# Performance work log

Hardware: AMD Instinct MI355X
Metric: run time of the kernel (lower is better)

## Reference

```python
import jax, jax.numpy as jnp
import numpy as np

HIDDEN = 2048
NUM_HEADS = 16
KEY_DIM = 1024      # hidden * expand_k (0.5)
VALUE_DIM = 2048    # hidden * expand_v (1.0)
HEAD_K = KEY_DIM // NUM_HEADS   # 64
HEAD_V = VALUE_DIM // NUM_HEADS # 128
EPS = 1e-5
B, T = 8, 4096


def _rmsnorm(x, w, eps=EPS):
    var = jnp.mean(jnp.square(x), axis=-1, keepdims=True)
    return x * jax.lax.rsqrt(var + eps) * w


def setup_inputs() -> dict:
    key = jax.random.key(0)
    ks = jax.random.split(key, 7)
    s = 1.0 / np.sqrt(HIDDEN)
    return {
        "hidden_states": jax.random.normal(ks[0], (B, T, HIDDEN), dtype=jnp.float32),
        "recurrent_state": jax.random.normal(ks[1], (B, NUM_HEADS, HEAD_K, HEAD_V), dtype=jnp.float32),
        "norm_w": jnp.ones((HIDDEN,), dtype=jnp.float32),
        "q_w": jax.random.uniform(ks[2], (KEY_DIM, HIDDEN), jnp.float32, -s, s),
        "v_norm_w": jnp.ones((HEAD_V,), dtype=jnp.float32),
        "o_w": jax.random.uniform(ks[3], (HIDDEN, VALUE_DIM), jnp.float32, -s, s),
        "gate_w": jax.random.uniform(ks[4], (HIDDEN, HIDDEN), jnp.float32, -s, s),
    }


def reference(hidden_states, recurrent_state, norm_w, q_w, v_norm_w, o_w, gate_w):
    x = _rmsnorm(hidden_states, norm_w)                       # (B,T,D)
    q = x @ q_w.T                                             # (B,T,KEY_DIM)
    q = q.reshape(*q.shape[:2], NUM_HEADS, HEAD_K)            # (B,T,H,K)
    # L2 normalize along last dim (F.normalize default eps=1e-12 on the norm)
    norm = jnp.maximum(jnp.linalg.norm(q, axis=-1, keepdims=True), 1e-12)
    q = q / norm
    o = jnp.einsum('bthk,bhkv->bthv', q, recurrent_state)     # (B,T,H,V)
    o = _rmsnorm(o, v_norm_w)
    o = o.reshape(*o.shape[:2], VALUE_DIM)                    # (B,T,VALUE_DIM)
    o = o @ o_w.T                                             # (B,T,D)
    gate = jax.nn.sigmoid(x @ gate_w.T)                       # (B,T,D)
    return gate * o
```

## Files before the change

### kernel.cpp

```cpp
#include <hip/hip_runtime.h>

typedef unsigned short u16;
typedef unsigned int u32;
typedef __attribute__((ext_vector_type(4))) float f32x4;
typedef __attribute__((ext_vector_type(8))) short short8;
typedef __attribute__((ext_vector_type(4))) short short4v;

#define HIDDEN 2048
#define NHEADS 16
#define KEYDIM 1024
#define VALDIM 2048
#define HEADK 64
#define HEADV 128
#define NBATCH 8
#define SEQ 4096
#define NTOK (NBATCH * SEQ)

__device__ __forceinline__ u16 f2bf(float f) {
  union { float f; u32 u; } c; c.f = f;
  u32 r = c.u + 0x7FFFu + ((c.u >> 16) & 1u);
  return (u16)(r >> 16);
}
__device__ __forceinline__ float bf2f(u16 h) {
  union { u32 u; float f; } c; c.u = ((u32)h) << 16;
  return c.f;
}

__global__ __launch_bounds__(256) void cast_bf16_k(const float* __restrict__ in,
                                                   u16* __restrict__ out, int n4) {
  int i = blockIdx.x * blockDim.x + threadIdx.x;
  if (i >= n4) return;
  f32x4 v = *(const f32x4*)(in + (size_t)i * 4);
  short4v o;
  o[0] = (short)f2bf(v[0]); o[1] = (short)f2bf(v[1]);
  o[2] = (short)f2bf(v[2]); o[3] = (short)f2bf(v[3]);
  *(short4v*)(out + (size_t)i * 4) = o;
}

__global__ __launch_bounds__(256) void rmsnorm_cast_k(const float* __restrict__ x,
                                                      const float* __restrict__ w,
                                                      u16* __restrict__ xb) {
  int r = blockIdx.x;
  int tid = threadIdx.x;
  const float* xp = x + (size_t)r * HIDDEN + tid * 8;
  f32x4 v0 = *(const f32x4*)xp;
  f32x4 v1 = *(const f32x4*)(xp + 4);
  float ss = v0[0]*v0[0]+v0[1]*v0[1]+v0[2]*v0[2]+v0[3]*v0[3]
           + v1[0]*v1[0]+v1[1]*v1[1]+v1[2]*v1[2]+v1[3]*v1[3];
  #pragma unroll
  for (int m = 32; m >= 1; m >>= 1) ss += __shfl_xor(ss, m);
  __shared__ float red[4];
  if ((tid & 63) == 0) red[tid >> 6] = ss;
  __syncthreads();
  float tot = red[0] + red[1] + red[2] + red[3];
  float inv = rsqrtf(tot * (1.0f / HIDDEN) + 1e-5f);
  const float* wp = w + tid * 8;
  f32x4 w0 = *(const f32x4*)wp;
  f32x4 w1 = *(const f32x4*)(wp + 4);
  short8 o;
  o[0] = (short)f2bf(v0[0] * inv * w0[0]);
  o[1] = (short)f2bf(v0[1] * inv * w0[1]);
  o[2] = (short)f2bf(v0[2] * inv * w0[2]);
  o[3] = (short)f2bf(v0[3] * inv * w0[3]);
  o[4] = (short)f2bf(v1[0] * inv * w1[0]);
  o[5] = (short)f2bf(v1[1] * inv * w1[1]);
  o[6] = (short)f2bf(v1[2] * inv * w1[2]);
  o[7] = (short)f2bf(v1[3] * inv * w1[3]);
  *(short8*)(xb + (size_t)r * HIDDEN + tid * 8) = o;
}


__device__ __forceinline__ void gload16(const u16* g, u16* l) {
  __builtin_amdgcn_global_load_lds((const __attribute__((address_space(1))) void*)g,
                                   (__attribute__((address_space(3))) void*)l, 16, 0, 0);
}

#define BUF_U16 16384
#define NBUF 4

template <int MODE>
__global__ __launch_bounds__(512, 2) void gemm256_k(const u16* __restrict__ A,
                                                    const u16* __restrict__ Bw,
                                                    void* __restrict__ Cptr,
                                                    int M, int N, int K) {
  extern __shared__ u16 lds[];
  const int tid = threadIdx.x;
  const int wid = tid >> 6;
  const int wm = wid >> 2;
  const int wn = wid & 3;
  const int l = tid & 63;
  const int lr = l & 15;
  const int kq = l >> 4;

  const int ntn = N >> 8;
  const int per = gridDim.x >> 3;
  const int b = blockIdx.x;
  const int s = (b & 7) * per + (b >> 3);
  const int mt = s / ntn;
  const int nt = s - mt * ntn;

  const u16* Ag = A + (size_t)mt * 256 * K;
  const u16* Bg = Bw + (size_t)nt * 256 * K;

  const int srow = tid >> 2;
  const int kel = (((tid & 3) ^ ((tid >> 3) & 3)) << 3);
  u16* dA0 = lds + tid * 8;
  u16* dA1 = lds + (512 + tid) * 8;
  u16* dB0 = lds + 8192 + tid * 8;
  u16* dB1 = lds + 8192 + (512 + tid) * 8;

  const int NT = K >> 5;

#define STAGE(t)                                                        \
  do {                                                                  \
    int _off = (int)(((t) & 3) * BUF_U16);                              \
    int _k0 = (t) << 5;                                                 \
    const u16* _as = Ag + (size_t)srow * K + _k0 + kel;                 \
    gload16(_as, dA0 + _off);                                           \
    gload16(_as + (size_t)128 * K, dA1 + _off);                         \
    const u16* _bs = Bg + (size_t)srow * K + _k0 + kel;                 \
    gload16(_bs, dB0 + _off);                                           \
    gload16(_bs + (size_t)128 * K, dB1 + _off);                         \
  } while (0)

  STAGE(0);
  STAGE(1);
  STAGE(2);

  f32x4 acc[8][4] = {};

  for (int t = 0; t < NT; ++t) {
    if (t + 2 < NT)      asm volatile("s_waitcnt vmcnt(8)" ::: "memory");
    else if (t + 1 < NT) asm volatile("s_waitcnt vmcnt(4)" ::: "memory");
    else                 asm volatile("s_waitcnt vmcnt(0)" ::: "memory");
    __builtin_amdgcn_s_barrier();
    asm volatile("" ::: "memory");
    __builtin_amdgcn_sched_barrier(0);

    if (t + 3 < NT) STAGE(t + 3);

    const u16* bufA = lds + (size_t)(t & 3) * BUF_U16;
    const u16* bufB = bufA + 8192;

    short8 bfr[4], afr[8];
    #pragma unroll
    for (int n = 0; n < 4; ++n) {
      int R = wn * 64 + n * 16 + lr;
      bfr[n] = *(const short8*)(bufB + R * 32 + ((kq ^ ((R >> 1) & 3)) << 3));
    }
    #pragma unroll
    for (int m = 0; m < 8; ++m) {
      int R = wm * 128 + m * 16 + lr;
      afr[m] = *(const short8*)(bufA + R * 32 + ((kq ^ ((R >> 1) & 3)) << 3));
    }
    __builtin_amdgcn_s_setprio(1);
    #pragma unroll
    for (int m = 0; m < 8; ++m) {
      #pragma unroll
      for (int n = 0; n < 4; ++n)
        acc[m][n] = __builtin_amdgcn_mfma_f32_16x16x32_bf16(afr[m], bfr[n], acc[m][n], 0, 0, 0);
    }
    __builtin_amdgcn_s_setprio(0);
  }
#undef STAGE

  const int rowB = mt * 256 + wm * 128 + kq * 4;
  const int colB = nt * 256 + wn * 64 + lr;
  #pragma unroll
  for (int m = 0; m < 8; ++m) {
    #pragma unroll
    for (int n = 0; n < 4; ++n) {
      #pragma unroll
      for (int j = 0; j < 4; ++j) {
        int row = rowB + m * 16 + j;
        int col = colB + n * 16;
        size_t idx = (size_t)row * N + col;
        float v = acc[m][n][j];
        if constexpr (MODE == 0) {
          ((u16*)Cptr)[idx] = f2bf(v);
        } else if constexpr (MODE == 1) {
          ((float*)Cptr)[idx] = 1.0f / (1.0f + __expf(-v));
        } else {
          float* O = (float*)Cptr;
          O[idx] = O[idx] * v;
        }
      }
    }
  }
}

__global__ __launch_bounds__(256) void glaread_k(const u16* __restrict__ q,
                                                 const float* __restrict__ S,
                                                 const float* __restrict__ vw,
                                                 u16* __restrict__ omid) {
  int bh = blockIdx.x;
  int b = bh >> 4, h = bh & 15;
  int tid = threadIdx.x;
  int w = tid >> 6, l = tid & 63;
  int lr = l & 15, kq = l >> 4;

  const float* Sp = S + (size_t)bh * HEADK * HEADV;
  short8 bfrag[8][2];
  #pragma unroll
  for (int n = 0; n < 8; ++n) {
    #pragma unroll
    for (int s = 0; s < 2; ++s) {
      #pragma unroll
      for (int i = 0; i < 8; ++i)
        bfrag[n][s][i] =
            (short)f2bf(Sp[(size_t)(s * 32 + kq * 8 + i) * HEADV + n * 16 + lr]);
    }
  }
  float vwn[8];
  #pragma unroll
  for (int n = 0; n < 8; ++n) vwn[n] = vw[n * 16 + lr];

  #pragma unroll 1
  for (int it = 0; it < 8; ++it) {
    int t0 = blockIdx.y * 512 + it * 64 + w * 16;
    const u16* qp = q + (size_t)(b * SEQ + t0 + lr) * KEYDIM + h * HEADK;
    short8 a0 = *(const short8*)(qp + kq * 8);
    short8 a1 = *(const short8*)(qp + 32 + kq * 8);

    float ss = 0.f;
    #pragma unroll
    for (int i = 0; i < 8; ++i) {
      float x0 = bf2f((u16)a0[i]), x1 = bf2f((u16)a1[i]);
      ss += x0 * x0 + x1 * x1;
    }
    ss += __shfl_xor(ss, 16);
    ss += __shfl_xor(ss, 32);
    float sc = 1.0f / fmaxf(sqrtf(ss), 1e-12f);

    short8 an0, an1;
    #pragma unroll
    for (int i = 0; i < 8; ++i) {
      an0[i] = (short)f2bf(bf2f((u16)a0[i]) * sc);
      an1[i] = (short)f2bf(bf2f((u16)a1[i]) * sc);
    }

    f32x4 acc[8] = {};
    #pragma unroll
    for (int n = 0; n < 8; ++n) {
      acc[n] = __builtin_amdgcn_mfma_f32_16x16x32_bf16(an0, bfrag[n][0], acc[n], 0, 0, 0);
      acc[n] = __builtin_amdgcn_mfma_f32_16x16x32_bf16(an1, bfrag[n][1], acc[n], 0, 0, 0);
    }

    float part[4] = {0.f, 0.f, 0.f, 0.f};
    #pragma unroll
    for (int n = 0; n < 8; ++n) {
      #pragma unroll
      for (int j = 0; j < 4; ++j) part[j] += acc[n][j] * acc[n][j];
    }
    #pragma unroll
    for (int msk = 1; msk <= 8; msk <<= 1) {
      #pragma unroll
      for (int j = 0; j < 4; ++j) part[j] += __shfl_xor(part[j], msk);
    }
    #pragma unroll
    for (int j = 0; j < 4; ++j) {
      float inv = rsqrtf(part[j] * (1.0f / HEADV) + 1e-5f);
      int tok = t0 + kq * 4 + j;
      u16* op = omid + (size_t)(b * SEQ + tok) * VALDIM + h * HEADV;
      #pragma unroll
      for (int n = 0; n < 8; ++n)
        op[n * 16 + lr] = f2bf(acc[n][j] * inv * vwn[n]);
    }
  }
}

extern "C" void kernel_launch(void* const* d_in, const int* in_sizes, int n_in,
                              void* d_out, int out_size, void* d_ws, size_t ws_size,
                              hipStream_t stream) {
  const float* hs = (const float*)d_in[0];
  const float* S  = (const float*)d_in[1];
  const float* nw = (const float*)d_in[2];
  const float* qw = (const float*)d_in[3];
  const float* vw = (const float*)d_in[4];
  const float* ow = (const float*)d_in[5];
  const float* gw = (const float*)d_in[6];
  float* out = (float*)d_out;

  u16* xb   = (u16*)d_ws;
  u16* q    = xb + (size_t)NTOK * HIDDEN;
  u16* qwb  = q + (size_t)NTOK * KEYDIM;
  u16* owb  = qwb + (size_t)KEYDIM * HIDDEN;
  u16* gwb  = owb + (size_t)HIDDEN * VALDIM;
  u16* omid = xb;

  const size_t LDSB = (size_t)NBUF * BUF_U16 * sizeof(u16);

  cast_bf16_k<<<(KEYDIM * HIDDEN / 4 + 255) / 256, 256, 0, stream>>>(qw, qwb, KEYDIM * HIDDEN / 4);
  cast_bf16_k<<<(HIDDEN * VALDIM / 4 + 255) / 256, 256, 0, stream>>>(ow, owb, HIDDEN * VALDIM / 4);
  cast_bf16_k<<<(HIDDEN * HIDDEN / 4 + 255) / 256, 256, 0, stream>>>(gw, gwb, HIDDEN * HIDDEN / 4);

  rmsnorm_cast_k<<<NTOK, 256, 0, stream>>>(hs, nw, xb);

  gemm256_k<0><<<dim3((NTOK / 256) * (KEYDIM / 256)), 512, LDSB, stream>>>(xb, qwb, q, NTOK, KEYDIM, HIDDEN);

  gemm256_k<1><<<dim3((NTOK / 256) * (HIDDEN / 256)), 512, LDSB, stream>>>(xb, gwb, out, NTOK, HIDDEN, HIDDEN);

  glaread_k<<<dim3(NBATCH * NHEADS, SEQ / 512), 256, 0, stream>>>(q, S, vw, omid);

  gemm256_k<2><<<dim3((NTOK / 256) * (HIDDEN / 256)), 512, LDSB, stream>>>(omid, owb, out, NTOK, HIDDEN, VALDIM);
}
```

Baseline: 0.9999 ms.

## Restructure GEMM main loop into 8-phase ping-pong schedule with 64-wide K tiles

Replaces the 4-buffer, 32-wide-K GEMM pipeline with a two-buffer, 64-wide-K scheme. Each K=128 iteration is split into eight phases, each issuing one quarter of the LDS fragment loads and global-to-LDS prefetches and then a barrier-bracketed MFMA block. The goal is to interleave memory traffic with MFMA work in a fixed schedule, in the style of the HipKittens 8-wave pattern. LDS rises to 128KB per block, which likely limits occupancy to one block per CU despite launch_bounds(512,2), and the added barriers raise synchronisation overhead.

```diff
diff --git a/kernel.cpp b/kernel.cpp
--- a/kernel.cpp
+++ b/kernel.cpp
@@ -75,14 +75,17 @@
                                    (__attribute__((address_space(3))) void*)l, 16, 0, 0);
 }
 
-#define BUF_U16 16384
-#define NBUF 4
+#define BAR()                                  \
+  do {                                         \
+    __builtin_amdgcn_s_barrier();              \
+    __builtin_amdgcn_sched_barrier(0);         \
+  } while (0)
 
 template <int MODE>
-__global__ __launch_bounds__(512, 2) void gemm256_k(const u16* __restrict__ A,
-                                                    const u16* __restrict__ Bw,
-                                                    void* __restrict__ Cptr,
-                                                    int M, int N, int K) {
+__global__ __launch_bounds__(512, 2) void gemm8p_k(const u16* __restrict__ A,
+                                                   const u16* __restrict__ Bw,
+                                                   void* __restrict__ Cptr,
+                                                   int M, int N, int K) {
   extern __shared__ u16 lds[];
   const int tid = threadIdx.x;
   const int wid = tid >> 6;
@@ -95,74 +98,115 @@
   const int ntn = N >> 8;
   const int per = gridDim.x >> 3;
   const int b = blockIdx.x;
-  const int s = (b & 7) * per + (b >> 3);
-  const int mt = s / ntn;
-  const int nt = s - mt * ntn;
-
-  const u16* Ag = A + (size_t)mt * 256 * K;
-  const u16* Bg = Bw + (size_t)nt * 256 * K;
-
-  const int srow = tid >> 2;
-  const int kel = (((tid & 3) ^ ((tid >> 3) & 3)) << 3);
-  u16* dA0 = lds + tid * 8;
-  u16* dA1 = lds + (512 + tid) * 8;
-  u16* dB0 = lds + 8192 + tid * 8;
-  u16* dB1 = lds + 8192 + (512 + tid) * 8;
-
-  const int NT = K >> 5;
-
-#define STAGE(t)                                                        \
-  do {                                                                  \
-    int _off = (int)(((t) & 3) * BUF_U16);                              \
-    int _k0 = (t) << 5;                                                 \
-    const u16* _as = Ag + (size_t)srow * K + _k0 + kel;                 \
-    gload16(_as, dA0 + _off);                                           \
-    gload16(_as + (size_t)128 * K, dA1 + _off);                         \
-    const u16* _bs = Bg + (size_t)srow * K + _k0 + kel;                 \
-    gload16(_bs, dB0 + _off);                                           \
-    gload16(_bs + (size_t)128 * K, dB1 + _off);                         \
+  const int sidx = (b & 7) * per + (b >> 3);
+  const int mt = sidx / ntn;
+  const int nt = sidx - mt * ntn;
+
+  const u16* Ag = A + (size_t)(mt * 256) * K;
+  const u16* Bg = Bw + (size_t)(nt * 256) * K;
+
+  const int srow = tid >> 3;
+  const int schunk = (tid & 7) ^ (srow & 7);
+
+#define STAGE_A(c, h)                                                          \
+  do {                                                                         \
+    const u16* _s = Ag + (size_t)((h) * 128 + srow) * K + ((c) << 6) + schunk * 8; \
+    u16* _d = lds + (((c) & 1) << 15) + (h) * 8192 + tid * 8;                  \
+    gload16(_s, _d);                                                           \
+    gload16(_s + (size_t)64 * K, _d + 4096);                                   \
   } while (0)
-
-  STAGE(0);
-  STAGE(1);
-  STAGE(2);
-
+#define STAGE_B(c, h)                                                          \
+  do {                                                                         \
+    const u16* _s = Bg + (size_t)((h) * 128 + srow) * K + ((c) << 6) + schunk * 8; \
+    u16* _d = lds + (((c) & 1) << 15) + 16384 + (h) * 8192 + tid * 8;          \
+    gload16(_s, _d);                                                           \
+    gload16(_s + (size_t)64 * K, _d + 4096);                                   \
+  } while (0)
+
+  const int c0s = (kq ^ (lr & 7)) << 3;
+  const int c1s = ((4 + kq) ^ (lr & 7)) << 3;
+  const int aRowBase = (wm * 128 + lr) * 64;
+  const int bRowBase = (wn * 64 + lr) * 64;
+
+  short8 afr[4][2];
+  short8 bfr[2][2][2];
   f32x4 acc[8][4] = {};
 
-  for (int t = 0; t < NT; ++t) {
-    if (t + 2 < NT)      asm volatile("s_waitcnt vmcnt(8)" ::: "memory");
-    else if (t + 1 < NT) asm volatile("s_waitcnt vmcnt(4)" ::: "memory");
-    else                 asm volatile("s_waitcnt vmcnt(0)" ::: "memory");
-    __builtin_amdgcn_s_barrier();
-    asm volatile("" ::: "memory");
-    __builtin_amdgcn_sched_barrier(0);
-
-    if (t + 3 < NT) STAGE(t + 3);
-
-    const u16* bufA = lds + (size_t)(t & 3) * BUF_U16;
-    const u16* bufB = bufA + 8192;
-
-    short8 bfr[4], afr[8];
-    #pragma unroll
-    for (int n = 0; n < 4; ++n) {
-      int R = wn * 64 + n * 16 + lr;
-      bfr[n] = *(const short8*)(bufB + R * 32 + ((kq ^ ((R >> 1) & 3)) << 3));
-    }
-    #pragma unroll
-    for (int m = 0; m < 8; ++m) {
-      int R = wm * 128 + m * 16 + lr;
-      afr[m] = *(const short8*)(bufA + R * 32 + ((kq ^ ((R >> 1) & 3)) << 3));
-    }
+  auto LDA = [&](int buf, int mh) {
+    #pragma unroll
+    for (int mi = 0; mi < 4; ++mi) {
+      const u16* p = lds + (buf << 15) + aRowBase + (mh * 64 + mi * 16) * 64;
+      afr[mi][0] = *(const short8*)(p + c0s);
+      afr[mi][1] = *(const short8*)(p + c1s);
+    }
+  };
+  auto LDB = [&](int buf, int nh) {
+    #pragma unroll
+    for (int ni = 0; ni < 2; ++ni) {
+      const u16* p = lds + (buf << 15) + 16384 + bRowBase + ((nh * 2 + ni) * 16) * 64;
+      bfr[nh][ni][0] = *(const short8*)(p + c0s);
+      bfr[nh][ni][1] = *(const short8*)(p + c1s);
+    }
+  };
+  auto MMA = [&](int mh, int nh) {
     __builtin_amdgcn_s_setprio(1);
     #pragma unroll
-    for (int m = 0; m < 8; ++m) {
-      #pragma unroll
-      for (int n = 0; n < 4; ++n)
-        acc[m][n] = __builtin_amdgcn_mfma_f32_16x16x32_bf16(afr[m], bfr[n], acc[m][n], 0, 0, 0);
+    for (int mi = 0; mi < 4; ++mi) {
+      #pragma unroll
+      for (int ni = 0; ni < 2; ++ni) {
+        int m = mh * 4 + mi, n = nh * 2 + ni;
+        acc[m][n] = __builtin_amdgcn_mfma_f32_16x16x32_bf16(afr[mi][0], bfr[nh][ni][0], acc[m][n], 0, 0, 0);
+        acc[m][n] = __builtin_amdgcn_mfma_f32_16x16x32_bf16(afr[mi][1], bfr[nh][ni][1], acc[m][n], 0, 0, 0);
+      }
     }
     __builtin_amdgcn_s_setprio(0);
+  };
+
+  STAGE_B(0, 0); STAGE_B(0, 1);
+  STAGE_A(0, 0); STAGE_A(0, 1);
+  STAGE_B(1, 0); STAGE_B(1, 1);
+  asm volatile("s_waitcnt vmcnt(4)" ::: "memory");
+  BAR();
+
+  const int NITER = K >> 7;
+  for (int i = 0; i < NITER; ++i) {
+    const int g = (i + 1 < NITER);
+    const int cA = 2 * i + 1, c2 = 2 * i + 2, c3 = 2 * i + 3;
+
+    LDA(0, 0); LDB(0, 0);
+    STAGE_A(cA, 0);
+    BAR(); MMA(0, 0); BAR();
+    LDB(0, 1);
+    STAGE_A(cA, 1);
+    BAR(); MMA(0, 1); BAR();
+    LDA(0, 1);
+    if (g) STAGE_B(c2, 0);
+    BAR(); MMA(1, 1); BAR();
+    if (g) {
+      STAGE_B(c2, 1);
+      asm volatile("s_waitcnt vmcnt(4)" ::: "memory");
+    } else {
+      asm volatile("s_waitcnt vmcnt(0)" ::: "memory");
+    }
+    BAR(); MMA(1, 0); BAR();
+
+    LDA(1, 0); LDB(1, 0);
+    if (g) STAGE_A(c2, 0);
+    BAR(); MMA(0, 0); BAR();
+    LDB(1, 1);
+    if (g) STAGE_A(c2, 1);
+    BAR(); MMA(0, 1); BAR();
+    LDA(1, 1);
+    if (g) STAGE_B(c3, 0);
+    BAR(); MMA(1, 1); BAR();
+    if (g) {
+      STAGE_B(c3, 1);
+      asm volatile("s_waitcnt vmcnt(4)" ::: "memory");
+    }
+    BAR(); MMA(1, 0); BAR();
   }
-#undef STAGE
+#undef STAGE_A
+#undef STAGE_B
 
   const int rowB = mt * 256 + wm * 128 + kq * 4;
   const int colB = nt * 256 + wn * 64 + lr;
@@ -288,7 +332,7 @@
   u16* gwb  = owb + (size_t)HIDDEN * VALDIM;
   u16* omid = xb;
 
-  const size_t LDSB = (size_t)NBUF * BUF_U16 * sizeof(u16);
+  const size_t LDSB = 131072;
 
   cast_bf16_k<<<(KEYDIM * HIDDEN / 4 + 255) / 256, 256, 0, stream>>>(qw, qwb, KEYDIM * HIDDEN / 4);
   cast_bf16_k<<<(HIDDEN * VALDIM / 4 + 255) / 256, 256, 0, stream>>>(ow, owb, HIDDEN * VALDIM / 4);
@@ -296,11 +340,11 @@
 
   rmsnorm_cast_k<<<NTOK, 256, 0, stream>>>(hs, nw, xb);
 
-  gemm256_k<0><<<dim3((NTOK / 256) * (KEYDIM / 256)), 512, LDSB, stream>>>(xb, qwb, q, NTOK, KEYDIM, HIDDEN);
-
-  gemm256_k<1><<<dim3((NTOK / 256) * (HIDDEN / 256)), 512, LDSB, stream>>>(xb, gwb, out, NTOK, HIDDEN, HIDDEN);
+  gemm8p_k<0><<<dim3((NTOK / 256) * (KEYDIM / 256)), 512, LDSB, stream>>>(xb, qwb, q, NTOK, KEYDIM, HIDDEN);
+
+  gemm8p_k<1><<<dim3((NTOK / 256) * (HIDDEN / 256)), 512, LDSB, stream>>>(xb, gwb, out, NTOK, HIDDEN, HIDDEN);
 
   glaread_k<<<dim3(NBATCH * NHEADS, SEQ / 512), 256, 0, stream>>>(q, S, vw, omid);
 
-  gemm256_k<2><<<dim3((NTOK / 256) * (HIDDEN / 256)), 512, LDSB, stream>>>(omid, owb, out, NTOK, HIDDEN, VALDIM);
-}
+  gemm8p_k<2><<<dim3((NTOK / 256) * (HIDDEN / 256)), 512, LDSB, stream>>>(omid, owb, out, NTOK, HIDDEN, VALDIM);
+}
```

After: 943.4 us. -5.7%, faster.

## Split GEMM K-step into two half-tile phases with interleaved staging and barriers

Applied to the files above, without the earlier changes.

Restructures the 256x256 bf16 GEMM main loop so each K-step runs in two phases of 16 MFMAs. Each phase loads only half of the A fragments (4 instead of 8 registers) and issues the A or B global-to-LDS stage for step c+3 between phases, with extra barriers in between. LDS offsets are precomputed once outside the loop. The intent is to cut register pressure and spread memory issue across the MFMA work for better overlap, at the cost of four barriers per K-step instead of one.

```diff
diff --git a/kernel.cpp b/kernel.cpp
--- a/kernel.cpp
+++ b/kernel.cpp
@@ -75,14 +75,17 @@
                                    (__attribute__((address_space(3))) void*)l, 16, 0, 0);
 }
 
-#define BUF_U16 16384
-#define NBUF 4
+#define BAR()                                  \
+  do {                                         \
+    __builtin_amdgcn_s_barrier();              \
+    __builtin_amdgcn_sched_barrier(0x0F);      \
+  } while (0)
 
 template <int MODE>
-__global__ __launch_bounds__(512, 2) void gemm256_k(const u16* __restrict__ A,
-                                                    const u16* __restrict__ Bw,
-                                                    void* __restrict__ Cptr,
-                                                    int M, int N, int K) {
+__global__ __launch_bounds__(512, 2) void gemm4r_k(const u16* __restrict__ A,
+                                                   const u16* __restrict__ Bw,
+                                                   void* __restrict__ Cptr,
+                                                   int M, int N, int K) {
   extern __shared__ u16 lds[];
   const int tid = threadIdx.x;
   const int wid = tid >> 6;
@@ -95,74 +98,95 @@
   const int ntn = N >> 8;
   const int per = gridDim.x >> 3;
   const int b = blockIdx.x;
-  const int s = (b & 7) * per + (b >> 3);
-  const int mt = s / ntn;
-  const int nt = s - mt * ntn;
-
-  const u16* Ag = A + (size_t)mt * 256 * K;
-  const u16* Bg = Bw + (size_t)nt * 256 * K;
+  const int sidx = (b & 7) * per + (b >> 3);
+  const int mt = sidx / ntn;
+  const int nt = sidx - mt * ntn;
+
+  const u16* Ag = A + (size_t)(mt * 256) * K;
+  const u16* Bg = Bw + (size_t)(nt * 256) * K;
 
   const int srow = tid >> 2;
   const int kel = (((tid & 3) ^ ((tid >> 3) & 3)) << 3);
-  u16* dA0 = lds + tid * 8;
-  u16* dA1 = lds + (512 + tid) * 8;
-  u16* dB0 = lds + 8192 + tid * 8;
-  u16* dB1 = lds + 8192 + (512 + tid) * 8;
+
+#define STAGE_A(c)                                               \
+  do {                                                           \
+    const u16* _s = Ag + (size_t)srow * K + ((c) << 5) + kel;    \
+    u16* _d = lds + (((c) & 3) << 14) + tid * 8;                 \
+    gload16(_s, _d);                                             \
+    gload16(_s + (size_t)128 * K, _d + 4096);                    \
+  } while (0)
+#define STAGE_B(c)                                               \
+  do {                                                           \
+    const u16* _s = Bg + (size_t)srow * K + ((c) << 5) + kel;    \
+    u16* _d = lds + (((c) & 3) << 14) + 8192 + tid * 8;          \
+    gload16(_s, _d);                                             \
+    gload16(_s + (size_t)128 * K, _d + 4096);                    \
+  } while (0)
+
+  int aoff[2][4], boff[4];
+  #pragma unroll
+  for (int mi = 0; mi < 4; ++mi) {
+    int R0 = wm * 128 + mi * 16 + lr;
+    aoff[0][mi] = R0 * 32 + ((kq ^ ((R0 >> 1) & 3)) << 3);
+    int R1 = R0 + 64;
+    aoff[1][mi] = R1 * 32 + ((kq ^ ((R1 >> 1) & 3)) << 3);
+  }
+  #pragma unroll
+  for (int n = 0; n < 4; ++n) {
+    int R = wn * 64 + n * 16 + lr;
+    boff[n] = 8192 + R * 32 + ((kq ^ ((R >> 1) & 3)) << 3);
+  }
+
+  short8 afr[4], bfr[4];
+  f32x4 acc[8][4] = {};
+
+  STAGE_A(0); STAGE_B(0);
+  STAGE_A(1); STAGE_B(1);
+  STAGE_A(2); STAGE_B(2);
+  asm volatile("s_waitcnt vmcnt(8)" ::: "memory");
+  BAR();
 
   const int NT = K >> 5;
-
-#define STAGE(t)                                                        \
-  do {                                                                  \
-    int _off = (int)(((t) & 3) * BUF_U16);                              \
-    int _k0 = (t) << 5;                                                 \
-    const u16* _as = Ag + (size_t)srow * K + _k0 + kel;                 \
-    gload16(_as, dA0 + _off);                                           \
-    gload16(_as + (size_t)128 * K, dA1 + _off);                         \
-    const u16* _bs = Bg + (size_t)srow * K + _k0 + kel;                 \
-    gload16(_bs, dB0 + _off);                                           \
-    gload16(_bs + (size_t)128 * K, dB1 + _off);                         \
-  } while (0)
-
-  STAGE(0);
-  STAGE(1);
-  STAGE(2);
-
-  f32x4 acc[8][4] = {};
-
-  for (int t = 0; t < NT; ++t) {
-    if (t + 2 < NT)      asm volatile("s_waitcnt vmcnt(8)" ::: "memory");
-    else if (t + 1 < NT) asm volatile("s_waitcnt vmcnt(4)" ::: "memory");
-    else                 asm volatile("s_waitcnt vmcnt(0)" ::: "memory");
-    __builtin_amdgcn_s_barrier();
-    asm volatile("" ::: "memory");
-    __builtin_amdgcn_sched_barrier(0);
-
-    if (t + 3 < NT) STAGE(t + 3);
-
-    const u16* bufA = lds + (size_t)(t & 3) * BUF_U16;
-    const u16* bufB = bufA + 8192;
-
-    short8 bfr[4], afr[8];
-    #pragma unroll
-    for (int n = 0; n < 4; ++n) {
-      int R = wn * 64 + n * 16 + lr;
-      bfr[n] = *(const short8*)(bufB + R * 32 + ((kq ^ ((R >> 1) & 3)) << 3));
-    }
-    #pragma unroll
-    for (int m = 0; m < 8; ++m) {
-      int R = wm * 128 + m * 16 + lr;
-      afr[m] = *(const short8*)(bufA + R * 32 + ((kq ^ ((R >> 1) & 3)) << 3));
-    }
+  #pragma unroll 1
+  for (int c = 0; c < NT; ++c) {
+    const u16* bufT = lds + ((c & 3) << 14);
+    const int g3 = (c + 3 < NT);
+
+    #pragma unroll
+    for (int n = 0; n < 4; ++n) bfr[n] = *(const short8*)(bufT + boff[n]);
+    #pragma unroll
+    for (int mi = 0; mi < 4; ++mi) afr[mi] = *(const short8*)(bufT + aoff[0][mi]);
+    if (g3) STAGE_A(c + 3);
+    BAR();
     __builtin_amdgcn_s_setprio(1);
     #pragma unroll
-    for (int m = 0; m < 8; ++m) {
+    for (int mi = 0; mi < 4; ++mi) {
       #pragma unroll
       for (int n = 0; n < 4; ++n)
-        acc[m][n] = __builtin_amdgcn_mfma_f32_16x16x32_bf16(afr[m], bfr[n], acc[m][n], 0, 0, 0);
+        acc[mi][n] = __builtin_amdgcn_mfma_f32_16x16x32_bf16(afr[mi], bfr[n], acc[mi][n], 0, 0, 0);
     }
     __builtin_amdgcn_s_setprio(0);
-  }
-#undef STAGE
+    BAR();
+
+    #pragma unroll
+    for (int mi = 0; mi < 4; ++mi) afr[mi] = *(const short8*)(bufT + aoff[1][mi]);
+    if (g3) STAGE_B(c + 3);
+    BAR();
+    __builtin_amdgcn_s_setprio(1);
+    #pragma unroll
+    for (int mi = 0; mi < 4; ++mi) {
+      #pragma unroll
+      for (int n = 0; n < 4; ++n)
+        acc[4 + mi][n] = __builtin_amdgcn_mfma_f32_16x16x32_bf16(afr[mi], bfr[n], acc[4 + mi][n], 0, 0, 0);
+    }
+    __builtin_amdgcn_s_setprio(0);
+    if (g3)               asm volatile("s_waitcnt vmcnt(8)" ::: "memory");
+    else if (c + 2 < NT)  asm volatile("s_waitcnt vmcnt(4)" ::: "memory");
+    else if (c + 1 < NT)  asm volatile("s_waitcnt vmcnt(0)" ::: "memory");
+    BAR();
+  }
+#undef STAGE_A
+#undef STAGE_B
 
   const int rowB = mt * 256 + wm * 128 + kq * 4;
   const int colB = nt * 256 + wn * 64 + lr;
@@ -288,7 +312,7 @@
   u16* gwb  = owb + (size_t)HIDDEN * VALDIM;
   u16* omid = xb;
 
-  const size_t LDSB = (size_t)NBUF * BUF_U16 * sizeof(u16);
+  const size_t LDSB = 131072;
 
   cast_bf16_k<<<(KEYDIM * HIDDEN / 4 + 255) / 256, 256, 0, stream>>>(qw, qwb, KEYDIM * HIDDEN / 4);
   cast_bf16_k<<<(HIDDEN * VALDIM / 4 + 255) / 256, 256, 0, stream>>>(ow, owb, HIDDEN * VALDIM / 4);
@@ -296,11 +320,11 @@
 
   rmsnorm_cast_k<<<NTOK, 256, 0, stream>>>(hs, nw, xb);
 
-  gemm256_k<0><<<dim3((NTOK / 256) * (KEYDIM / 256)), 512, LDSB, stream>>>(xb, qwb, q, NTOK, KEYDIM, HIDDEN);
-
-  gemm256_k<1><<<dim3((NTOK / 256) * (HIDDEN / 256)), 512, LDSB, stream>>>(xb, gwb, out, NTOK, HIDDEN, HIDDEN);
+  gemm4r_k<0><<<dim3((NTOK / 256) * (KEYDIM / 256)), 512, LDSB, stream>>>(xb, qwb, q, NTOK, KEYDIM, HIDDEN);
+
+  gemm4r_k<1><<<dim3((NTOK / 256) * (HIDDEN / 256)), 512, LDSB, stream>>>(xb, gwb, out, NTOK, HIDDEN, HIDDEN);
 
   glaread_k<<<dim3(NBATCH * NHEADS, SEQ / 512), 256, 0, stream>>>(q, S, vw, omid);
 
-  gemm256_k<2><<<dim3((NTOK / 256) * (HIDDEN / 256)), 512, LDSB, stream>>>(omid, owb, out, NTOK, HIDDEN, VALDIM);
-}
+  gemm4r_k<2><<<dim3((NTOK / 256) * (HIDDEN / 256)), 512, LDSB, stream>>>(omid, owb, out, NTOK, HIDDEN, VALDIM);
+}
```

Result: no change. 1.010 ms (+1.0%).

## Replace 256x256 GEMM tiles with 128x128 tiles and triple-buffered ring pipeline

Applied to the files above, without the earlier changes.

The GEMM kernel moves from 256x256 tiles with 512 threads and 4 LDS buffers to 128x128 tiles with 256 threads, 3 LDS buffers rotated as a ring, and up to 3 blocks per CU. LDS fragment offsets are precomputed, and fragment loads are issued before the next prefetch with a single barrier per k-step. Smaller tiles give more blocks and better occupancy and load balance, but each block re-reads more global data per FLOP and the per-wave MFMA work per barrier halves.

```diff
diff --git a/kernel.cpp b/kernel.cpp
--- a/kernel.cpp
+++ b/kernel.cpp
@@ -75,99 +75,101 @@
                                    (__attribute__((address_space(3))) void*)l, 16, 0, 0);
 }
 
-#define BUF_U16 16384
-#define NBUF 4
-
 template <int MODE>
-__global__ __launch_bounds__(512, 2) void gemm256_k(const u16* __restrict__ A,
-                                                    const u16* __restrict__ Bw,
-                                                    void* __restrict__ Cptr,
-                                                    int M, int N, int K) {
+__global__ __launch_bounds__(256, 3) void gemm128r_k(const u16* __restrict__ A,
+                                                     const u16* __restrict__ Bw,
+                                                     void* __restrict__ Cptr,
+                                                     int M, int N, int K) {
   extern __shared__ u16 lds[];
   const int tid = threadIdx.x;
   const int wid = tid >> 6;
-  const int wm = wid >> 2;
-  const int wn = wid & 3;
+  const int wm = wid >> 1;
+  const int wn = wid & 1;
   const int l = tid & 63;
   const int lr = l & 15;
   const int kq = l >> 4;
 
-  const int ntn = N >> 8;
+  const int ntn = N >> 7;
   const int per = gridDim.x >> 3;
   const int b = blockIdx.x;
-  const int s = (b & 7) * per + (b >> 3);
-  const int mt = s / ntn;
-  const int nt = s - mt * ntn;
-
-  const u16* Ag = A + (size_t)mt * 256 * K;
-  const u16* Bg = Bw + (size_t)nt * 256 * K;
+  const int sidx = (b & 7) * per + (b >> 3);
+  const int mt = sidx / ntn;
+  const int nt = sidx - mt * ntn;
+
+  const u16* Ag = A + (size_t)(mt * 128) * K;
+  const u16* Bg = Bw + (size_t)(nt * 128) * K;
 
   const int srow = tid >> 2;
   const int kel = (((tid & 3) ^ ((tid >> 3) & 3)) << 3);
-  u16* dA0 = lds + tid * 8;
-  u16* dA1 = lds + (512 + tid) * 8;
-  u16* dB0 = lds + 8192 + tid * 8;
-  u16* dB1 = lds + 8192 + (512 + tid) * 8;
+
+#define STAGE(c, bi)                                                  \
+  do {                                                                \
+    const u16* _sa = Ag + (size_t)srow * K + ((c) << 5) + kel;        \
+    u16* _d = lds + (bi) * 8192 + tid * 8;                            \
+    gload16(_sa, _d);                                                 \
+    gload16(_sa + (size_t)64 * K, _d + 2048);                         \
+    const u16* _sb = Bg + (size_t)srow * K + ((c) << 5) + kel;        \
+    gload16(_sb, _d + 4096);                                          \
+    gload16(_sb + (size_t)64 * K, _d + 6144);                         \
+  } while (0)
+
+  int aoff[4], boff[4];
+  #pragma unroll
+  for (int mi = 0; mi < 4; ++mi) {
+    int R = wm * 64 + mi * 16 + lr;
+    aoff[mi] = R * 32 + ((kq ^ ((R >> 1) & 3)) << 3);
+  }
+  #pragma unroll
+  for (int n = 0; n < 4; ++n) {
+    int R = wn * 64 + n * 16 + lr;
+    boff[n] = 4096 + R * 32 + ((kq ^ ((R >> 1) & 3)) << 3);
+  }
+
+  f32x4 acc[4][4] = {};
+
+  STAGE(0, 0);
+  STAGE(1, 1);
+  asm volatile("s_waitcnt vmcnt(4)" ::: "memory");
+  __builtin_amdgcn_s_barrier();
 
   const int NT = K >> 5;
-
-#define STAGE(t)                                                        \
-  do {                                                                  \
-    int _off = (int)(((t) & 3) * BUF_U16);                              \
-    int _k0 = (t) << 5;                                                 \
-    const u16* _as = Ag + (size_t)srow * K + _k0 + kel;                 \
-    gload16(_as, dA0 + _off);                                           \
-    gload16(_as + (size_t)128 * K, dA1 + _off);                         \
-    const u16* _bs = Bg + (size_t)srow * K + _k0 + kel;                 \
-    gload16(_bs, dB0 + _off);                                           \
-    gload16(_bs + (size_t)128 * K, dB1 + _off);                         \
-  } while (0)
-
-  STAGE(0);
-  STAGE(1);
-  STAGE(2);
-
-  f32x4 acc[8][4] = {};
-
-  for (int t = 0; t < NT; ++t) {
-    if (t + 2 < NT)      asm volatile("s_waitcnt vmcnt(8)" ::: "memory");
-    else if (t + 1 < NT) asm volatile("s_waitcnt vmcnt(4)" ::: "memory");
-    else                 asm volatile("s_waitcnt vmcnt(0)" ::: "memory");
+  int cur = 0, nxt = 1, stg = 2;
+  #pragma unroll 1
+  for (int c = 0; c < NT; ++c) {
+    const u16* bufT = lds + cur * 8192;
+    short8 afr[4], bfr[4];
+    #pragma unroll
+    for (int mi = 0; mi < 4; ++mi) afr[mi] = *(const short8*)(bufT + aoff[mi]);
+    #pragma unroll
+    for (int n = 0; n < 4; ++n)   bfr[n] = *(const short8*)(bufT + boff[n]);
+
+    if (c + 2 < NT) {
+      STAGE(c + 2, stg);
+      asm volatile("s_waitcnt vmcnt(4) lgkmcnt(0)" ::: "memory");
+    } else if (c + 1 < NT) {
+      asm volatile("s_waitcnt vmcnt(0) lgkmcnt(0)" ::: "memory");
+    } else {
+      asm volatile("s_waitcnt lgkmcnt(0)" ::: "memory");
+    }
     __builtin_amdgcn_s_barrier();
-    asm volatile("" ::: "memory");
-    __builtin_amdgcn_sched_barrier(0);
-
-    if (t + 3 < NT) STAGE(t + 3);
-
-    const u16* bufA = lds + (size_t)(t & 3) * BUF_U16;
-    const u16* bufB = bufA + 8192;
-
-    short8 bfr[4], afr[8];
-    #pragma unroll
-    for (int n = 0; n < 4; ++n) {
-      int R = wn * 64 + n * 16 + lr;
-      bfr[n] = *(const short8*)(bufB + R * 32 + ((kq ^ ((R >> 1) & 3)) << 3));
-    }
-    #pragma unroll
-    for (int m = 0; m < 8; ++m) {
-      int R = wm * 128 + m * 16 + lr;
-      afr[m] = *(const short8*)(bufA + R * 32 + ((kq ^ ((R >> 1) & 3)) << 3));
-    }
+
     __builtin_amdgcn_s_setprio(1);
     #pragma unroll
-    for (int m = 0; m < 8; ++m) {
+    for (int mi = 0; mi < 4; ++mi) {
       #pragma unroll
       for (int n = 0; n < 4; ++n)
-        acc[m][n] = __builtin_amdgcn_mfma_f32_16x16x32_bf16(afr[m], bfr[n], acc[m][n], 0, 0, 0);
+        acc[mi][n] = __builtin_amdgcn_mfma_f32_16x16x32_bf16(afr[mi], bfr[n], acc[mi][n], 0, 0, 0);
     }
     __builtin_amdgcn_s_setprio(0);
+
+    int t = cur; cur = nxt; nxt = stg; stg = t;
   }
 #undef STAGE
 
-  const int rowB = mt * 256 + wm * 128 + kq * 4;
-  const int colB = nt * 256 + wn * 64 + lr;
-  #pragma unroll
-  for (int m = 0; m < 8; ++m) {
+  const int rowB = mt * 128 + wm * 64 + kq * 4;
+  const int colB = nt * 128 + wn * 64 + lr;
+  #pragma unroll
+  for (int m = 0; m < 4; ++m) {
     #pragma unroll
     for (int n = 0; n < 4; ++n) {
       #pragma unroll
@@ -288,7 +290,7 @@
   u16* gwb  = owb + (size_t)HIDDEN * VALDIM;
   u16* omid = xb;
 
-  const size_t LDSB = (size_t)NBUF * BUF_U16 * sizeof(u16);
+  const size_t LDSB = 49152;
 
   cast_bf16_k<<<(KEYDIM * HIDDEN / 4 + 255) / 256, 256, 0, stream>>>(qw, qwb, KEYDIM * HIDDEN / 4);
   cast_bf16_k<<<(HIDDEN * VALDIM / 4 + 255) / 256, 256, 0, stream>>>(ow, owb, HIDDEN * VALDIM / 4);
@@ -296,11 +298,11 @@
 
   rmsnorm_cast_k<<<NTOK, 256, 0, stream>>>(hs, nw, xb);
 
-  gemm256_k<0><<<dim3((NTOK / 256) * (KEYDIM / 256)), 512, LDSB, stream>>>(xb, qwb, q, NTOK, KEYDIM, HIDDEN);
-
-  gemm256_k<1><<<dim3((NTOK / 256) * (HIDDEN / 256)), 512, LDSB, stream>>>(xb, gwb, out, NTOK, HIDDEN, HIDDEN);
+  gemm128r_k<0><<<dim3((NTOK / 128) * (KEYDIM / 128)), 256, LDSB, stream>>>(xb, qwb, q, NTOK, KEYDIM, HIDDEN);
+
+  gemm128r_k<1><<<dim3((NTOK / 128) * (HIDDEN / 128)), 256, LDSB, stream>>>(xb, gwb, out, NTOK, HIDDEN, HIDDEN);
 
   glaread_k<<<dim3(NBATCH * NHEADS, SEQ / 512), 256, 0, stream>>>(q, S, vw, omid);
 
-  gemm256_k<2><<<dim3((NTOK / 256) * (HIDDEN / 256)), 512, LDSB, stream>>>(omid, owb, out, NTOK, HIDDEN, VALDIM);
-}
+  gemm128r_k<2><<<dim3((NTOK / 128) * (HIDDEN / 128)), 256, LDSB, stream>>>(omid, owb, out, NTOK, HIDDEN, VALDIM);
+}
```

After: 1.141 ms. 1.14x slower.
